# Optimization experiments

Hardware: AMD Instinct MI355X
Metric: run time of the kernel (lower is better)

Reference implementation:

```python
import jax, jax.numpy as jnp
import numpy as np


def setup_inputs() -> dict:
    key = jax.random.key(0)
    ks = jax.random.split(key, 9)
    B, L, D, H, E = 8, 2048, 1024, 256, 8
    Hg = D // 4
    s = 0.02
    return {
        "x": jax.random.normal(ks[0], (B, L, D), dtype=jnp.float32),
        "wg1": jax.random.normal(ks[1], (D, Hg), dtype=jnp.float32) * s,
        "bg1": jax.random.normal(ks[2], (Hg,), dtype=jnp.float32) * s,
        "wg2": jax.random.normal(ks[3], (Hg, E), dtype=jnp.float32) * s,
        "bg2": jax.random.normal(ks[4], (E,), dtype=jnp.float32) * s,
        "w1": jax.random.normal(ks[5], (E, D, H), dtype=jnp.float32) * (1.0 / np.sqrt(D)),
        "b1": jax.random.normal(ks[6], (E, H), dtype=jnp.float32) * s,
        "w2": jax.random.normal(ks[7], (E, H, D), dtype=jnp.float32) * (1.0 / np.sqrt(H)),
        "b2": jax.random.normal(ks[8], (E, D), dtype=jnp.float32) * s,
        "k": 2,
    }


def reference(x, wg1, bg1, wg2, bg2, w1, b1, w2, b2, k):
    B, L, D = x.shape
    xt = x.reshape(-1, D)                       # [T, D] tokens
    T = xt.shape[0]
    # gating MLP: Linear -> GELU(exact, matches torch nn.GELU) -> Linear -> softmax
    logits = jax.nn.gelu(xt @ wg1 + bg1, approximate=False) @ wg2 + bg2  # [T, E]
    scores = jax.nn.softmax(logits, axis=-1)
    top_v, top_i = jax.lax.top_k(scores, k)     # [T, k]
    # dense gate matrix (equivalent to compute_gating's scatter); zeros for non-top-k
    gates = jnp.zeros_like(scores).at[jnp.arange(T)[:, None], top_i].set(top_v)  # [T, E]

    # grouped-GEMM MoE: y[t] = sum_e gates[t,e] * (gelu(x[t] @ W1_e + b1_e) @ W2_e + b2_e)
    # scan over the fixed, small expert axis; gates zero out non-selected experts,
    # giving math identical to the sort/dispatch + per-expert torch.mm loop.
    def body(acc, we):
        w1e, b1e, w2e, b2e, ge = we
        h = jax.nn.gelu(xt @ w1e + b1e, approximate=False)  # [T, H]
        o = h @ w2e + b2e                                    # [T, D]
        return acc + ge[:, None] * o, None

    y, _ = jax.lax.scan(body, jnp.zeros_like(xt), (w1, b1, w2, b2, gates.T))
    return y.reshape(B, L, D)
```

## Files before the change

kernel.cpp:

```cpp
#include <hip/hip_runtime.h>

typedef unsigned short u16;
typedef __attribute__((ext_vector_type(8))) short bf16x8;
typedef __attribute__((ext_vector_type(4))) float f32x4;
typedef __attribute__((ext_vector_type(4))) u16 u16x4;

#define T_TOK 16384
#define D_DIM 1024
#define NE 8
#define MAXP 33792

__device__ __forceinline__ u16 f2bf(float f) {
  union { float f; unsigned int u; } c; c.f = f;
  unsigned int u = c.u;
  u += 0x7fffu + ((u >> 16) & 1u);
  return (u16)(u >> 16);
}

__device__ __forceinline__ float bf2f(u16 v) {
  union { unsigned int u; float f; } c; c.u = ((unsigned int)v) << 16;
  return c.f;
}

__device__ __forceinline__ float gelu_exact(float u) {
  return 0.5f * u * (1.0f + erff(u * 0.70710678118654752f));
}

__device__ __forceinline__ void gld16(const void* g, void* l) {
  __builtin_amdgcn_global_load_lds(
      (const __attribute__((address_space(1))) unsigned int*)g,
      (__attribute__((address_space(3))) unsigned int*)l, 16, 0, 0);
}


__device__ __forceinline__ void stage_tile_swz(u16* lds, const char* g0, size_t stride,
                                               int wid, int lane) {
  const int rg = lane >> 3;
  const int cs = ((lane & 7) ^ rg) * 16;
  const char* g = g0 + (size_t)(wid * 8 + rg) * stride + cs;
  char* l = (char*)lds + wid * 1024;
  #pragma unroll
  for (int c = 0; c < 4; ++c)
    gld16(g + (size_t)(32 * c) * stride, l + c * 4096);
}

__device__ __forceinline__ void stage_a128_8w(u16* lds, const char* g0, size_t stride,
                                              int wid, int lane) {
  const int rg = lane >> 3;
  const int cs = ((lane & 7) ^ rg) * 16;
  const char* g = g0 + (size_t)(wid * 16 + rg) * stride + cs;
  char* l = (char*)lds + wid * 2048;
  gld16(g, l);
  gld16(g + (size_t)8 * stride, l + 1024);
}

__device__ __forceinline__ void stage_b256_8w(u16* lds, const char* g0, size_t stride,
                                              int wid, int lane) {
  const int rg = lane >> 3;
  const int cs = ((lane & 7) ^ rg) * 16;
  const char* g = g0 + (size_t)(wid * 32 + rg) * stride + cs;
  char* l = (char*)lds + wid * 4096;
  #pragma unroll
  for (int c = 0; c < 4; ++c)
    gld16(g + (size_t)(8 * c) * stride, l + c * 1024);
}

__device__ __forceinline__ bf16x8 rd_swz(const u16* lds, int row, int colu16) {
  const int byte = (row * 128 + colu16 * 2) ^ ((row & 7) << 4);
  return *(const bf16x8*)((const char*)lds + byte);
}

__device__ __forceinline__ void mma_step_swz(const u16* As, const u16* Bs, f32x4 acc[4][4],
                                             int wm, int wn, int lane) {
  const int r = lane & 15, kq = (lane >> 4) * 8;
  #pragma unroll
  for (int ks = 0; ks < 2; ++ks) {
    const int col = ks * 32 + kq;
    bf16x8 a[4], b[4];
    #pragma unroll
    for (int mf = 0; mf < 4; ++mf)
      a[mf] = rd_swz(As, wm * 64 + mf * 16 + r, col);
    #pragma unroll
    for (int nf = 0; nf < 4; ++nf)
      b[nf] = rd_swz(Bs, wn * 64 + nf * 16 + r, col);
    #pragma unroll
    for (int mf = 0; mf < 4; ++mf)
      #pragma unroll
      for (int nf = 0; nf < 4; ++nf)
        acc[mf][nf] = __builtin_amdgcn_mfma_f32_16x16x32_bf16(a[mf], b[nf], acc[mf][nf], 0, 0, 0);
  }
}

__device__ __forceinline__ void mma_64x128_swz(const u16* As, const u16* Bs, f32x4 acc[2][4],
                                               int wm, int wn, int lane) {
  const int r = lane & 15, kq = (lane >> 4) * 8;
  #pragma unroll
  for (int ks = 0; ks < 2; ++ks) {
    const int col = ks * 32 + kq;
    bf16x8 a[2], b[4];
    #pragma unroll
    for (int mf = 0; mf < 2; ++mf)
      a[mf] = rd_swz(As, wm * 32 + mf * 16 + r, col);
    #pragma unroll
    for (int nf = 0; nf < 4; ++nf)
      b[nf] = rd_swz(Bs, wn * 64 + nf * 16 + r, col);
    #pragma unroll
    for (int mf = 0; mf < 2; ++mf)
      #pragma unroll
      for (int nf = 0; nf < 4; ++nf)
        acc[mf][nf] = __builtin_amdgcn_mfma_f32_16x16x32_bf16(a[mf], b[nf], acc[mf][nf], 0, 0, 0);
  }
}

__device__ __forceinline__ void stage_b64x32(u16* lds, const u16* mat, int rowbase,
                                             int k0, int wid, int lane) {
  const int row = wid * 16 + (lane >> 2);
  const char* g = (const char*)(mat + (size_t)(rowbase + row) * 1024 + k0 + (lane & 3) * 8);
  char* l = (char*)lds + wid * 1024;
  gld16(g, l);
}

__device__ __forceinline__ void stage_b32(u16* lds, const u16* mat, int rowbase,
                                          int k0, int wid, int lane) {
  const char* g0 = (const char*)(mat + (size_t)rowbase * 1024 + k0);
  #pragma unroll
  for (int c = 0; c < 2; ++c) {
    const int row = c * 64 + wid * 16 + (lane >> 2);
    const char* g = g0 + (size_t)row * 2048 + (size_t)((lane & 3) * 16);
    char* l = (char*)lds + c * 4096 + wid * 1024;
    gld16(g, l);
  }
}

__device__ __forceinline__ int find_expert(const int* offs, int p0) {
  int e = 0;
  #pragma unroll
  for (int q = 1; q < NE; ++q) if (p0 >= offs[q]) e = q;
  return e;
}

__global__ __launch_bounds__(256) void cvt_hilo_x_kernel(const float* __restrict__ x,
                                                         u16* __restrict__ xh,
                                                         u16* __restrict__ xl) {
  const int i = (blockIdx.x * 256 + threadIdx.x) * 4;
  float4 v = *(const float4*)(x + i);
  float vv[4] = {v.x, v.y, v.z, v.w};
  u16x4 h, l;
  u16 hh[4], ll[4];
  #pragma unroll
  for (int q = 0; q < 4; ++q) { hh[q] = f2bf(vv[q]); ll[q] = f2bf(vv[q] - bf2f(hh[q])); }
  h.x = hh[0]; h.y = hh[1]; h.z = hh[2]; h.w = hh[3];
  l.x = ll[0]; l.y = ll[1]; l.z = ll[2]; l.w = ll[3];
  *(u16x4*)(xh + i) = h;
  *(u16x4*)(xl + i) = l;
}

__global__ __launch_bounds__(256) void transpose_cvt_kernel(const float* __restrict__ in,
                                                            u16* __restrict__ out,
                                                            int R, int C) {
  __shared__ u16 t[32][36];
  const int e = blockIdx.z;
  const int r0 = blockIdx.x * 32, c0 = blockIdx.y * 32;
  const int tid = threadIdx.x;
  {
    const int r = tid >> 3, cq = (tid & 7) * 4;
    float4 v = *(const float4*)(in + ((size_t)e * R + r0 + r) * C + c0 + cq);
    t[r][cq + 0] = f2bf(v.x); t[r][cq + 1] = f2bf(v.y);
    t[r][cq + 2] = f2bf(v.z); t[r][cq + 3] = f2bf(v.w);
  }
  __syncthreads();
  {
    const int c = tid >> 3, rq = (tid & 7) * 4;
    u16x4 o;
    o.x = t[rq + 0][c]; o.y = t[rq + 1][c]; o.z = t[rq + 2][c]; o.w = t[rq + 3][c];
    *(u16x4*)(out + ((size_t)e * C + c0 + c) * R + r0 + rq) = o;
  }
}

__global__ __launch_bounds__(256) void transpose_hilo_kernel(const float* __restrict__ in,
                                                             u16* __restrict__ out_hi,
                                                             u16* __restrict__ out_lo,
                                                             int R, int C) {
  __shared__ u16 th[32][36];
  __shared__ u16 tl[32][36];
  const int r0 = blockIdx.x * 32, c0 = blockIdx.y * 32;
  const int tid = threadIdx.x;
  {
    const int r = tid >> 3, cq = (tid & 7) * 4;
    float4 v = *(const float4*)(in + (size_t)(r0 + r) * C + c0 + cq);
    float vv[4] = {v.x, v.y, v.z, v.w};
    #pragma unroll
    for (int i = 0; i < 4; ++i) {
      u16 h = f2bf(vv[i]);
      th[r][cq + i] = h;
      tl[r][cq + i] = f2bf(vv[i] - bf2f(h));
    }
  }
  __syncthreads();
  {
    const int c = tid >> 3, rq = (tid & 7) * 4;
    u16x4 oh, ol;
    oh.x = th[rq + 0][c]; oh.y = th[rq + 1][c]; oh.z = th[rq + 2][c]; oh.w = th[rq + 3][c];
    ol.x = tl[rq + 0][c]; ol.y = tl[rq + 1][c]; ol.z = tl[rq + 2][c]; ol.w = tl[rq + 3][c];
    *(u16x4*)(out_hi + (size_t)(c0 + c) * R + r0 + rq) = oh;
    *(u16x4*)(out_lo + (size_t)(c0 + c) * R + r0 + rq) = ol;
  }
}

__global__ __launch_bounds__(256) void gating_mfma_kernel(
    const u16* __restrict__ xh, const u16* __restrict__ xl,
    const u16* __restrict__ wg1t_hi, const u16* __restrict__ wg1t_lo,
    float* __restrict__ p_buf) {
  __shared__ u16 Ah[64 * 32], Al[64 * 32];
  __shared__ u16 Bh[128 * 32], Bl[128 * 32];
  const int tid = threadIdx.x, lane = tid & 63, wid = tid >> 6;
  const int t0 = blockIdx.x * 64, n0 = blockIdx.y * 128;
  const int kh = blockIdx.z, kbeg = kh * 512;
  const int wm = wid >> 1, wn = wid & 1;

  f32x4 acc[2][4];
  #pragma unroll
  for (int i = 0; i < 2; ++i)
    #pragma unroll
    for (int j = 0; j < 4; ++j) acc[i][j] = (f32x4){0.f, 0.f, 0.f, 0.f};

  for (int kt = 0; kt < 16; ++kt) {
    const int k0 = kbeg + kt * 32;
    __syncthreads();
    stage_b64x32(Ah, xh, t0, k0, wid, lane);
    stage_b64x32(Al, xl, t0, k0, wid, lane);
    stage_b32(Bh, wg1t_hi, n0, k0, wid, lane);
    stage_b32(Bl, wg1t_lo, n0, k0, wid, lane);
    __syncthreads();
    const int r = lane & 15, ko = (lane >> 4) * 8;
    bf16x8 ah[2], al[2];
    #pragma unroll
    for (int mf = 0; mf < 2; ++mf) {
      const int ro = (wm * 32 + mf * 16 + r) * 32 + ko;
      ah[mf] = *(const bf16x8*)&Ah[ro];
      al[mf] = *(const bf16x8*)&Al[ro];
    }
    #pragma unroll
    for (int nf = 0; nf < 4; ++nf) {
      const int ro = (wn * 64 + nf * 16 + r) * 32 + ko;
      bf16x8 bh = *(const bf16x8*)&Bh[ro];
      bf16x8 bl = *(const bf16x8*)&Bl[ro];
      #pragma unroll
      for (int mf = 0; mf < 2; ++mf) {
        acc[mf][nf] = __builtin_amdgcn_mfma_f32_16x16x32_bf16(ah[mf], bh, acc[mf][nf], 0, 0, 0);
        acc[mf][nf] = __builtin_amdgcn_mfma_f32_16x16x32_bf16(ah[mf], bl, acc[mf][nf], 0, 0, 0);
        acc[mf][nf] = __builtin_amdgcn_mfma_f32_16x16x32_bf16(al[mf], bh, acc[mf][nf], 0, 0, 0);
      }
    }
  }

  #pragma unroll
  for (int mf = 0; mf < 2; ++mf)
    #pragma unroll
    for (int rr = 0; rr < 4; ++rr) {
      const int lt = wm * 32 + mf * 16 + ((lane >> 4) << 2) + rr;
      #pragma unroll
      for (int nf = 0; nf < 4; ++nf) {
        const int ln = wn * 64 + nf * 16 + (lane & 15);
        p_buf[((size_t)kh * T_TOK + t0 + lt) * 256 + n0 + ln] = acc[mf][nf][rr];
      }
    }
}

__global__ __launch_bounds__(256) void gating_p2_kernel(
    const float* __restrict__ p_buf, const float* __restrict__ bg1,
    const float* __restrict__ wg2, const float* __restrict__ bg2,
    int* __restrict__ top_i, float2* __restrict__ top_g) {
  const int tid = threadIdx.x;
  const int tn = tid & 31, tm = tid >> 5;
  const int t0 = blockIdx.x * 32;

  float bb[8];
  {
    float4 ba = *(const float4*)&bg1[tn * 4];
    float4 bc = *(const float4*)&bg1[128 + tn * 4];
    bb[0] = ba.x; bb[1] = ba.y; bb[2] = ba.z; bb[3] = ba.w;
    bb[4] = bc.x; bb[5] = bc.y; bb[6] = bc.z; bb[7] = bc.w;
  }

  float hv[4][8];
  #pragma unroll
  for (int i = 0; i < 4; ++i) {
    const size_t t = t0 + tm * 4 + i;
    const float* pa = &p_buf[t * 256];
    const float* pb = &p_buf[((size_t)T_TOK + t) * 256];
    float4 a0 = *(const float4*)&pa[tn * 4];
    float4 a1 = *(const float4*)&pa[128 + tn * 4];
    float4 b0 = *(const float4*)&pb[tn * 4];
    float4 b1 = *(const float4*)&pb[128 + tn * 4];
    hv[i][0] = gelu_exact(a0.x + b0.x + bb[0]);
    hv[i][1] = gelu_exact(a0.y + b0.y + bb[1]);
    hv[i][2] = gelu_exact(a0.z + b0.z + bb[2]);
    hv[i][3] = gelu_exact(a0.w + b0.w + bb[3]);
    hv[i][4] = gelu_exact(a1.x + b1.x + bb[4]);
    hv[i][5] = gelu_exact(a1.y + b1.y + bb[5]);
    hv[i][6] = gelu_exact(a1.z + b1.z + bb[6]);
    hv[i][7] = gelu_exact(a1.w + b1.w + bb[7]);
  }

  float part[4][8];
  #pragma unroll
  for (int i = 0; i < 4; ++i)
    #pragma unroll
    for (int e = 0; e < 8; ++e) part[i][e] = 0.f;
  #pragma unroll
  for (int j = 0; j < 8; ++j) {
    const int col = (j < 4) ? (tn * 4 + j) : (128 + tn * 4 + (j - 4));
    float4 wa = *(const float4*)&wg2[col * 8];
    float4 wb = *(const float4*)&wg2[col * 8 + 4];
    float we[8] = {wa.x, wa.y, wa.z, wa.w, wb.x, wb.y, wb.z, wb.w};
    #pragma unroll
    for (int i = 0; i < 4; ++i)
      #pragma unroll
      for (int e = 0; e < 8; ++e) part[i][e] += hv[i][j] * we[e];
  }
  #pragma unroll
  for (int mask = 1; mask < 32; mask <<= 1)
    #pragma unroll
    for (int i = 0; i < 4; ++i)
      #pragma unroll
      for (int e = 0; e < 8; ++e) part[i][e] += __shfl_xor(part[i][e], mask);

  if (tn < 4) {
    float lg[8];
    #pragma unroll
    for (int i = 0; i < 4; ++i)
      if (tn == i) {
        #pragma unroll
        for (int e = 0; e < 8; ++e) lg[e] = part[i][e];
      }
    #pragma unroll
    for (int e = 0; e < 8; ++e) lg[e] += bg2[e];
    float m = lg[0];
    #pragma unroll
    for (int e = 1; e < 8; ++e) m = fmaxf(m, lg[e]);
    float ex[8], s = 0.f;
    #pragma unroll
    for (int e = 0; e < 8; ++e) { ex[e] = expf(lg[e] - m); s += ex[e]; }
    int i1 = 0;
    #pragma unroll
    for (int e = 1; e < 8; ++e) if (lg[e] > lg[i1]) i1 = e;
    int i2 = (i1 == 0) ? 1 : 0;
    #pragma unroll
    for (int e = 0; e < 8; ++e) if (e != i1 && lg[e] > lg[i2]) i2 = e;
    float inv = 1.f / s;
    const int t = t0 + tm * 4 + tn;
    top_i[t] = i1 | (i2 << 8);
    top_g[t] = make_float2(ex[i1] * inv, ex[i2] * inv);
  }
}

__global__ __launch_bounds__(256) void hist_kernel(const int* __restrict__ top_i,
                                                   int* __restrict__ hist) {
  __shared__ int h[NE];
  const int tid = threadIdx.x;
  if (tid < NE) h[tid] = 0;
  __syncthreads();
  const int ti = top_i[blockIdx.x * 256 + tid];
  atomicAdd(&h[ti & 255], 1);
  atomicAdd(&h[ti >> 8], 1);
  __syncthreads();
  if (tid < NE) hist[blockIdx.x * NE + tid] = h[tid];
}

__global__ __launch_bounds__(64) void scan_kernel(const int* __restrict__ hist,
                                                  int* __restrict__ cnt,
                                                  int* __restrict__ offs,
                                                  int* __restrict__ cbase) {
  __shared__ int tot[NE], off_s[NE];
  const int tid = threadIdx.x;
  if (tid < NE) {
    int s = 0;
    for (int c = 0; c < 64; ++c) s += hist[c * NE + tid];
    tot[tid] = s; cnt[tid] = s;
  }
  __syncthreads();
  if (tid == 0) {
    int o = 0;
    #pragma unroll
    for (int e = 0; e < NE; ++e) { off_s[e] = o; o += (tot[e] + 127) & ~127; }
  }
  __syncthreads();
  if (tid < NE) {
    offs[tid] = off_s[tid];
    int r = off_s[tid];
    for (int c = 0; c < 64; ++c) { cbase[c * NE + tid] = r; r += hist[c * NE + tid]; }
  }
}

__global__ __launch_bounds__(256) void fill_kernel(
    const int* __restrict__ top_i, const int* __restrict__ cbase,
    int* __restrict__ tok_list, int* __restrict__ pos1, int* __restrict__ pos2) {
  __shared__ int lcnt[NE];
  const int tid = threadIdx.x;
  if (tid < NE) lcnt[tid] = 0;
  __syncthreads();
  const int t = blockIdx.x * 256 + tid;
  const int ti = top_i[t];
  const int i1 = ti & 255, i2 = ti >> 8;
  const int r1 = atomicAdd(&lcnt[i1], 1);
  const int r2 = atomicAdd(&lcnt[i2], 1);
  const int p1 = cbase[blockIdx.x * NE + i1] + r1;
  const int p2 = cbase[blockIdx.x * NE + i2] + r2;
  tok_list[p1] = t; tok_list[p2] = t;
  pos1[t] = p1; pos2[t] = p2;
}

__global__ __launch_bounds__(256) void expert_h_kernel(
    const u16* __restrict__ xb, const u16* __restrict__ w1t,
    const float* __restrict__ b1, const int* __restrict__ tok_list,
    const int* __restrict__ cnt, const int* __restrict__ offs,
    u16* __restrict__ h_c) {
  __shared__ u16 As[64 * 64];
  __shared__ u16 Bs[128 * 64];
  __shared__ float b1_s[128];
  const int e = blockIdx.z;
  const int nblk = (cnt[e] + 63) >> 6;
  if ((int)blockIdx.x >= nblk) return;
  const int tid = threadIdx.x, lane = tid & 63, wid = tid >> 6;
  const int base = offs[e] + blockIdx.x * 64;
  const int n0 = blockIdx.y * 128;
  const int wm = wid >> 1, wn = wid & 1;

  if (tid < 128) b1_s[tid] = b1[e * 256 + n0 + tid];

  int tk[2];
  #pragma unroll
  for (int c = 0; c < 2; ++c)
    tk[c] = tok_list[base + (wid * 2 + c) * 8 + (lane >> 3)];

  f32x4 acc[2][4];
  #pragma unroll
  for (int i = 0; i < 2; ++i)
    #pragma unroll
    for (int j = 0; j < 4; ++j) acc[i][j] = (f32x4){0.f, 0.f, 0.f, 0.f};

  const char* Bb = (const char*)w1t + ((size_t)e * 256 + n0) * 2048;
  const int cb = ((lane & 7) ^ ((lane >> 3) & 7)) * 16;
  for (int kt = 0; kt < 16; ++kt) {
    __syncthreads();
    {
      char* l = (char*)As + wid * 2048;
      #pragma unroll
      for (int c = 0; c < 2; ++c)
        gld16((const char*)xb + (size_t)tk[c] * 2048 + kt * 128 + cb, l + c * 1024);
    }
    stage_tile_swz(Bs, Bb + kt * 128, 2048, wid, lane);
    __syncthreads();
    mma_64x128_swz(As, Bs, acc, wm, wn, lane);
  }

  #pragma unroll
  for (int mf = 0; mf < 2; ++mf)
    #pragma unroll
    for (int rr = 0; rr < 4; ++rr) {
      const int lt = wm * 32 + mf * 16 + ((lane >> 4) << 2) + rr;
      #pragma unroll
      for (int nf = 0; nf < 4; ++nf) {
        const int ln = wn * 64 + nf * 16 + (lane & 15);
        float u = acc[mf][nf][rr] + b1_s[ln];
        h_c[(size_t)(base + lt) * 256 + n0 + ln] = f2bf(gelu_exact(u));
      }
    }
}

__global__ __launch_bounds__(512) void moe_out_kernel(
    const u16* __restrict__ h_c, const u16* __restrict__ w2t,
    const float* __restrict__ b2, const int* __restrict__ cnt,
    const int* __restrict__ offs, u16* __restrict__ o_c) {
  __shared__ u16 As[128 * 64];
  __shared__ u16 Bs[256 * 64];
  const int tid = threadIdx.x, lane = tid & 63, wid = tid >> 6;
  const int base = blockIdx.x * 128;
  const int e = find_expert(offs, base);
  if (base >= offs[e] + ((cnt[e] + 127) & ~127)) return;
  const int n0 = blockIdx.y * 256;
  const int wm = wid >> 2, wn = wid & 3;
  const int r = lane & 15, kq = (lane >> 4) * 8;

  f32x4 acc[4][4];
  #pragma unroll
  for (int i = 0; i < 4; ++i)
    #pragma unroll
    for (int j = 0; j < 4; ++j) acc[i][j] = (f32x4){0.f, 0.f, 0.f, 0.f};

  const char* Ab = (const char*)h_c + (size_t)base * 512;
  const char* Bb = (const char*)w2t + ((size_t)e * D_DIM + n0) * 512;
  #pragma unroll 1
  for (int kt = 0; kt < 4; ++kt) {
    __syncthreads();
    stage_a128_8w(As, Ab + kt * 128, 512, wid, lane);
    stage_b256_8w(Bs, Bb + kt * 128, 512, wid, lane);
    __syncthreads();
    #pragma unroll
    for (int ks = 0; ks < 2; ++ks) {
      const int col = ks * 32 + kq;
      bf16x8 a[4], b[4];
      #pragma unroll
      for (int mf = 0; mf < 4; ++mf)
        a[mf] = rd_swz(As, wm * 64 + mf * 16 + r, col);
      #pragma unroll
      for (int nf = 0; nf < 4; ++nf)
        b[nf] = rd_swz(Bs, wn * 64 + nf * 16 + r, col);
      #pragma unroll
      for (int mf = 0; mf < 4; ++mf)
        #pragma unroll
        for (int nf = 0; nf < 4; ++nf)
          acc[mf][nf] = __builtin_amdgcn_mfma_f32_16x16x32_bf16(a[mf], b[nf], acc[mf][nf], 0, 0, 0);
    }
  }

  #pragma unroll
  for (int nf = 0; nf < 4; ++nf) {
    const int ln = wn * 64 + nf * 16 + (lane & 15);
    const float bv = b2[(size_t)e * 1024 + n0 + ln];
    #pragma unroll
    for (int mf = 0; mf < 4; ++mf)
      #pragma unroll
      for (int rr = 0; rr < 4; ++rr) {
        const int lt = wm * 64 + mf * 16 + ((lane >> 4) << 2) + rr;
        o_c[(size_t)(base + lt) * 1024 + n0 + ln] = f2bf(acc[mf][nf][rr] + bv);
      }
  }
}

__global__ __launch_bounds__(256) void gather_kernel(
    const u16* __restrict__ o_c, const int* __restrict__ pos1,
    const int* __restrict__ pos2, const float2* __restrict__ top_g,
    float* __restrict__ y) {
  const int t = blockIdx.x;
  const int p1 = pos1[t], p2 = pos2[t];
  const float2 g = top_g[t];
  const int c = threadIdx.x * 4;
  u16x4 a = *(const u16x4*)&o_c[(size_t)p1 * 1024 + c];
  u16x4 b = *(const u16x4*)&o_c[(size_t)p2 * 1024 + c];
  float4 o;
  o.x = g.x * bf2f(a.x) + g.y * bf2f(b.x);
  o.y = g.x * bf2f(a.y) + g.y * bf2f(b.y);
  o.z = g.x * bf2f(a.z) + g.y * bf2f(b.z);
  o.w = g.x * bf2f(a.w) + g.y * bf2f(b.w);
  *(float4*)&y[(size_t)t * 1024 + c] = o;
}

extern "C" void kernel_launch(void* const* d_in, const int* in_sizes, int n_in,
                              void* d_out, int out_size, void* d_ws, size_t ws_size,
                              hipStream_t stream) {
  (void)in_sizes; (void)n_in; (void)out_size; (void)ws_size;
  const float* x   = (const float*)d_in[0];
  const float* wg1 = (const float*)d_in[1];
  const float* bg1 = (const float*)d_in[2];
  const float* wg2 = (const float*)d_in[3];
  const float* bg2 = (const float*)d_in[4];
  const float* w1  = (const float*)d_in[5];
  const float* b1  = (const float*)d_in[6];
  const float* w2  = (const float*)d_in[7];
  const float* b2  = (const float*)d_in[8];
  float* y = (float*)d_out;

  char* ws = (char*)d_ws;
  u16* xb   = (u16*)(ws);
  u16* w1t  = (u16*)(ws + 33554432);
  u16* w2t  = (u16*)(ws + 37748736);
  char* M   = ws + 41943040;
  int*    cnt      = (int*)(M);
  int*    offs     = (int*)(M + 64);
  int*    hist     = (int*)(M + 128);
  int*    cbase    = (int*)(M + 2304);
  int*    tok_list = (int*)(M + 4608);
  int*    top_i    = (int*)(M + 139776);
  float2* top_g    = (float2*)(M + 205312);
  int*    pos1     = (int*)(M + 336384);
  int*    pos2     = (int*)(M + 401920);
  u16* h_c = (u16*)(ws + 42467328);
  u16* o_c = (u16*)(ws + 59768832);
  float* p_buf   = (float*)(ws + 59768832);
  u16*   wg1t_hi = (u16*)(ws + 93323264);
  u16*   wg1t_lo = (u16*)(ws + 93847552);
  u16*   xl      = (u16*)(ws + 94371840);

  hipMemsetAsync(tok_list, 0, 135168, stream);
  cvt_hilo_x_kernel<<<16384, 256, 0, stream>>>(x, xb, xl);
  transpose_cvt_kernel<<<dim3(32, 8, 8), 256, 0, stream>>>(w1, w1t, 1024, 256);
  transpose_cvt_kernel<<<dim3(8, 32, 8), 256, 0, stream>>>(w2, w2t, 256, 1024);
  transpose_hilo_kernel<<<dim3(32, 8), 256, 0, stream>>>(wg1, wg1t_hi, wg1t_lo, 1024, 256);
  gating_mfma_kernel<<<dim3(256, 2, 2), 256, 0, stream>>>(xb, xl, wg1t_hi, wg1t_lo, p_buf);
  gating_p2_kernel<<<512, 256, 0, stream>>>(p_buf, bg1, wg2, bg2, top_i, top_g);
  hist_kernel<<<64, 256, 0, stream>>>(top_i, hist);
  scan_kernel<<<1, 64, 0, stream>>>(hist, cnt, offs, cbase);
  fill_kernel<<<64, 256, 0, stream>>>(top_i, cbase, tok_list, pos1, pos2);
  expert_h_kernel<<<dim3(256, 2, 8), 256, 0, stream>>>(xb, w1t, b1, tok_list, cnt, offs, h_c);
  moe_out_kernel<<<dim3(264, 4), 512, 0, stream>>>(h_c, w2t, b2, cnt, offs, o_c);
  gather_kernel<<<16384, 256, 0, stream>>>(o_c, pos1, pos2, top_g, y);
}
```

Before: 191.5 us.

## Fuse gate-weighted combine into expert output GEMM via atomic scatter-add

The second expert GEMM now multiplies each output row by its token's gate weight and atomically adds it straight into the fp32 output, using per-slot token and gate lists written by the fill kernel. This removes the bf16 intermediate o_c buffer and the separate gather kernel, along with their full write and read of the expert outputs. In exchange the output must be zeroed with a memset first, and the epilogue issues scattered fp32 atomic adds with poorly coalesced per-element access. Padding slots carry zero gates and token 0, so they add zeros to row 0.

```diff
diff --git a/kernel.cpp b/kernel.cpp
--- a/kernel.cpp
+++ b/kernel.cpp
@@ -68,27 +68,6 @@
 __device__ __forceinline__ bf16x8 rd_swz(const u16* lds, int row, int colu16) {
   const int byte = (row * 128 + colu16 * 2) ^ ((row & 7) << 4);
   return *(const bf16x8*)((const char*)lds + byte);
-}
-
-__device__ __forceinline__ void mma_step_swz(const u16* As, const u16* Bs, f32x4 acc[4][4],
-                                             int wm, int wn, int lane) {
-  const int r = lane & 15, kq = (lane >> 4) * 8;
-  #pragma unroll
-  for (int ks = 0; ks < 2; ++ks) {
-    const int col = ks * 32 + kq;
-    bf16x8 a[4], b[4];
-    #pragma unroll
-    for (int mf = 0; mf < 4; ++mf)
-      a[mf] = rd_swz(As, wm * 64 + mf * 16 + r, col);
-    #pragma unroll
-    for (int nf = 0; nf < 4; ++nf)
-      b[nf] = rd_swz(Bs, wn * 64 + nf * 16 + r, col);
-    #pragma unroll
-    for (int mf = 0; mf < 4; ++mf)
-      #pragma unroll
-      for (int nf = 0; nf < 4; ++nf)
-        acc[mf][nf] = __builtin_amdgcn_mfma_f32_16x16x32_bf16(a[mf], b[nf], acc[mf][nf], 0, 0, 0);
-  }
 }
 
 __device__ __forceinline__ void mma_64x128_swz(const u16* As, const u16* Bs, f32x4 acc[2][4],
@@ -395,20 +374,22 @@
 
 __global__ __launch_bounds__(256) void fill_kernel(
     const int* __restrict__ top_i, const int* __restrict__ cbase,
-    int* __restrict__ tok_list, int* __restrict__ pos1, int* __restrict__ pos2) {
+    const float2* __restrict__ top_g, int* __restrict__ tok_list,
+    float* __restrict__ g_list) {
   __shared__ int lcnt[NE];
   const int tid = threadIdx.x;
   if (tid < NE) lcnt[tid] = 0;
   __syncthreads();
   const int t = blockIdx.x * 256 + tid;
   const int ti = top_i[t];
+  const float2 g = top_g[t];
   const int i1 = ti & 255, i2 = ti >> 8;
   const int r1 = atomicAdd(&lcnt[i1], 1);
   const int r2 = atomicAdd(&lcnt[i2], 1);
   const int p1 = cbase[blockIdx.x * NE + i1] + r1;
   const int p2 = cbase[blockIdx.x * NE + i2] + r2;
   tok_list[p1] = t; tok_list[p2] = t;
-  pos1[t] = p1; pos2[t] = p2;
+  g_list[p1] = g.x; g_list[p2] = g.y;
 }
 
 __global__ __launch_bounds__(256) void expert_h_kernel(
@@ -472,9 +453,12 @@
 __global__ __launch_bounds__(512) void moe_out_kernel(
     const u16* __restrict__ h_c, const u16* __restrict__ w2t,
     const float* __restrict__ b2, const int* __restrict__ cnt,
-    const int* __restrict__ offs, u16* __restrict__ o_c) {
+    const int* __restrict__ offs, const int* __restrict__ tok_list,
+    const float* __restrict__ g_list, float* __restrict__ y) {
   __shared__ u16 As[128 * 64];
   __shared__ u16 Bs[256 * 64];
+  __shared__ int tok_s[128];
+  __shared__ float g_s[128];
   const int tid = threadIdx.x, lane = tid & 63, wid = tid >> 6;
   const int base = blockIdx.x * 128;
   const int e = find_expert(offs, base);
@@ -482,6 +466,11 @@
   const int n0 = blockIdx.y * 256;
   const int wm = wid >> 2, wn = wid & 3;
   const int r = lane & 15, kq = (lane >> 4) * 8;
+
+  if (tid < 128) {
+    tok_s[tid] = tok_list[base + tid];
+    g_s[tid] = g_list[base + tid];
+  }
 
   f32x4 acc[4][4];
   #pragma unroll
@@ -524,27 +513,10 @@
       #pragma unroll
       for (int rr = 0; rr < 4; ++rr) {
         const int lt = wm * 64 + mf * 16 + ((lane >> 4) << 2) + rr;
-        o_c[(size_t)(base + lt) * 1024 + n0 + ln] = f2bf(acc[mf][nf][rr] + bv);
+        const float v = (acc[mf][nf][rr] + bv) * g_s[lt];
+        atomicAdd(&y[(size_t)tok_s[lt] * 1024 + n0 + ln], v);
       }
   }
-}
-
-__global__ __launch_bounds__(256) void gather_kernel(
-    const u16* __restrict__ o_c, const int* __restrict__ pos1,
-    const int* __restrict__ pos2, const float2* __restrict__ top_g,
-    float* __restrict__ y) {
-  const int t = blockIdx.x;
-  const int p1 = pos1[t], p2 = pos2[t];
-  const float2 g = top_g[t];
-  const int c = threadIdx.x * 4;
-  u16x4 a = *(const u16x4*)&o_c[(size_t)p1 * 1024 + c];
-  u16x4 b = *(const u16x4*)&o_c[(size_t)p2 * 1024 + c];
-  float4 o;
-  o.x = g.x * bf2f(a.x) + g.y * bf2f(b.x);
-  o.y = g.x * bf2f(a.y) + g.y * bf2f(b.y);
-  o.z = g.x * bf2f(a.z) + g.y * bf2f(b.z);
-  o.w = g.x * bf2f(a.w) + g.y * bf2f(b.w);
-  *(float4*)&y[(size_t)t * 1024 + c] = o;
 }
 
 extern "C" void kernel_launch(void* const* d_in, const int* in_sizes, int n_in,
@@ -574,16 +546,16 @@
   int*    tok_list = (int*)(M + 4608);
   int*    top_i    = (int*)(M + 139776);
   float2* top_g    = (float2*)(M + 205312);
-  int*    pos1     = (int*)(M + 336384);
-  int*    pos2     = (int*)(M + 401920);
+  float*  g_list   = (float*)(M + 336384);
   u16* h_c = (u16*)(ws + 42467328);
-  u16* o_c = (u16*)(ws + 59768832);
   float* p_buf   = (float*)(ws + 59768832);
   u16*   wg1t_hi = (u16*)(ws + 93323264);
   u16*   wg1t_lo = (u16*)(ws + 93847552);
   u16*   xl      = (u16*)(ws + 94371840);
 
   hipMemsetAsync(tok_list, 0, 135168, stream);
+  hipMemsetAsync(g_list, 0, 135168, stream);
+  hipMemsetAsync(y, 0, (size_t)T_TOK * D_DIM * 4, stream);
   cvt_hilo_x_kernel<<<16384, 256, 0, stream>>>(x, xb, xl);
   transpose_cvt_kernel<<<dim3(32, 8, 8), 256, 0, stream>>>(w1, w1t, 1024, 256);
   transpose_cvt_kernel<<<dim3(8, 32, 8), 256, 0, stream>>>(w2, w2t, 256, 1024);
@@ -592,8 +564,7 @@
   gating_p2_kernel<<<512, 256, 0, stream>>>(p_buf, bg1, wg2, bg2, top_i, top_g);
   hist_kernel<<<64, 256, 0, stream>>>(top_i, hist);
   scan_kernel<<<1, 64, 0, stream>>>(hist, cnt, offs, cbase);
-  fill_kernel<<<64, 256, 0, stream>>>(top_i, cbase, tok_list, pos1, pos2);
+  fill_kernel<<<64, 256, 0, stream>>>(top_i, cbase, top_g, tok_list, g_list);
   expert_h_kernel<<<dim3(256, 2, 8), 256, 0, stream>>>(xb, w1t, b1, tok_list, cnt, offs, h_c);
-  moe_out_kernel<<<dim3(264, 4), 512, 0, stream>>>(h_c, w2t, b2, cnt, offs, o_c);
-  gather_kernel<<<16384, 256, 0, stream>>>(o_c, pos1, pos2, top_g, y);
-}
+  moe_out_kernel<<<dim3(264, 4), 512, 0, stream>>>(h_c, w2t, b2, cnt, offs, tok_list, g_list, y);
+}
```

Result: slower. 349.5 us (+82.5%).
